# Kernel tuning notes

Measured on AMD Instinct MI355X. Metric: run time of the kernel, lower is better.

## Reference

```python
import jax, jax.numpy as jnp
import numpy as np
from jax import lax

H = 2048          # hidden_size
NAH = 16          # num attn heads
AHD = H // NAH    # 128
NFH = 4           # num lact (fast-weight) heads
FHD = H // NFH    # 512 = d_in = d_out
DH = FHD          # d_h = d_in * inter_multi (1.0)
WIN = 1024        # sliding window
CHUNK = 512       # lact chunk size
B, S = 2, 2048
ROPE_BASE = 500000.0
EPS = 1e-6
BASE_LR_INV = 0.001 + float(np.log(-np.expm1(-0.001)))  # inv_softplus(1e-3)


def rms_norm(x, w):
    return x * lax.rsqrt(jnp.mean(x * x, axis=-1, keepdims=True) + EPS) * w


def silu(x):
    return x * jax.nn.sigmoid(x)


def silu_backprop(dy, x):
    sg = jax.nn.sigmoid(x)
    return dy * sg * (1.0 + x * (1.0 - sg))


def apply_rope(q, k):
    # q,k: [b,s,h,d]; non-interleaved (half-split) rotary, matching flash-attn RotaryEmbedding
    d = q.shape[-1]
    inv_freq = 1.0 / (ROPE_BASE ** (jnp.arange(0, d, 2, dtype=jnp.float32) / d))
    t = jnp.arange(q.shape[1], dtype=jnp.float32)
    freqs = jnp.outer(t, inv_freq)                       # [s, d/2]
    cos = jnp.cos(freqs)[None, :, None, :]
    sin = jnp.sin(freqs)[None, :, None, :]
    def rot(x):
        x1, x2 = jnp.split(x, 2, axis=-1)
        return jnp.concatenate([x1 * cos - x2 * sin, x2 * cos + x1 * sin], axis=-1)
    return rot(q), rot(k)


def sliding_window_attn(q, k, v):
    # [b,s,h,d]; causal sliding-window attention
    s = q.shape[1]
    scale = 1.0 / np.sqrt(q.shape[-1])
    i = jnp.arange(s)[:, None]
    j = jnp.arange(s)[None, :]
    mask = (j <= i) & (i - j < WIN)                      # [s,s]
    scores = jnp.einsum('bihd,bjhd->bhij', q, k) * scale
    scores = jnp.where(mask[None, None], scores, -jnp.inf)
    p = jax.nn.softmax(scores, axis=-1)
    return jnp.einsum('bhij,bjhd->bihd', p, v)


def setup_inputs() -> dict:
    key = jax.random.key(0)
    ks = jax.random.split(key, 10)
    def n(k, shape, scale):
        return jax.random.normal(k, shape, dtype=jnp.float32) * scale
    return {
        'hidden_states': n(ks[0], (B, S, H), 1.0),
        'attn_qkv_w': n(ks[1], (3 * H, H), 0.02),
        'attn_o_w': n(ks[2], (H, H), 0.02),
        'q_norm_w': jnp.ones((H,), jnp.float32),
        'k_norm_w': jnp.ones((H,), jnp.float32),
        'mlp_norm_w': jnp.ones((H,), jnp.float32),
        'mlp_qkv_w': n(ks[3], (3 * NFH * FHD, H), 0.02),
        'mlp_o_w': n(ks[4], (H, NFH * FHD), 0.02),
        'lr_w': n(ks[5], (3 * NFH, H), 0.02),
        'lr_b': jnp.zeros((3 * NFH,), jnp.float32),
        'w0': n(ks[6], (NFH, DH, FHD), 1.0 / np.sqrt(FHD)),
        'w1': n(ks[7], (NFH, FHD, DH), 1.0 / np.sqrt(DH)),
        'w2': n(ks[8], (NFH, DH, FHD), 1.0 / np.sqrt(FHD)),
        'ttt_norm_w': jnp.ones((FHD,), jnp.float32),
    }


def _forward(hidden_states, attn_qkv_w, attn_o_w, q_norm_w, k_norm_w, mlp_norm_w,
             mlp_qkv_w, mlp_o_w, lr_w, lr_b, w0, w1, w2, ttt_norm_w):
    b, s, _ = hidden_states.shape
    # ---- sliding window attention (token mixer) ----
    qkv = hidden_states @ attn_qkv_w.T
    q, k, v = jnp.split(qkv, 3, axis=-1)
    q = rms_norm(q, q_norm_w)
    k = rms_norm(k, k_norm_w)
    q = q.reshape(b, s, NAH, AHD)
    k = k.reshape(b, s, NAH, AHD)
    v = v.reshape(b, s, NAH, AHD)
    q, k = apply_rope(q, k)
    o = sliding_window_attn(q, k, v)
    attn_out = o.reshape(b, s, H) @ attn_o_w.T

    # ---- TTT-MLP SwiGLU fast-weight channel mixer after SWA ----
    x = rms_norm(attn_out, mlp_norm_w)
    fqkv = x @ mlp_qkv_w.T
    fq, fk, fv = jnp.split(fqkv, 3, axis=-1)
    fq, fk, fv = silu(fq), silu(fk), silu(fv)
    fq = fq.reshape(b, s, NFH, FHD)
    fk = fk.reshape(b, s, NFH, FHD)
    fv = fv.reshape(b, s, NFH, FHD)
    fq = fq / jnp.clip(jnp.linalg.norm(fq, axis=-1, keepdims=True), 1e-6)
    fk = fk / jnp.clip(jnp.linalg.norm(fk, axis=-1, keepdims=True), 1e-6)

    # per-token lrs (mamba parameterization: softplus(proj + inv_softplus(base_lr)))
    lr = jax.nn.softplus(x @ lr_w.T + lr_b + BASE_LR_INV)   # [b,s,3*NFH]
    l0, l1, l2 = jnp.split(lr, 3, axis=-1)                  # each [b,s,NFH]

    nc = s // CHUNK
    def chunkify(t):  # [b,s,h,d] -> [nc,b,h,c,d]
        return t.reshape(b, nc, CHUNK, t.shape[2], t.shape[3]).transpose(1, 0, 3, 2, 4)
    qs = chunkify(fq)
    ks_ = chunkify(fk)
    vs = chunkify(fv)
    l0s = chunkify(l0[..., None])
    l1s = chunkify(l1[..., None])
    l2s = chunkify(l2[..., None])

    w0b = jnp.broadcast_to(w0[None], (b,) + w0.shape)
    w1b = jnp.broadcast_to(w1[None], (b,) + w1.shape)
    w2b = jnp.broadcast_to(w2[None], (b,) + w2.shape)

    def step(carry, inp):
        cw0, cw1, cw2 = carry
        qc, kc, vc, lr0, lr1, lr2 = inp   # qc/kc/vc: [b,h,c,d]; lr*: [b,h,c,1]
        # apply current fast weights to queries of this chunk (apply-then-update)
        gq = jnp.einsum('bhed,bhcd->bhce', cw0, qc)
        hq = silu(gq) * jnp.einsum('bhed,bhcd->bhce', cw2, qc)
        oc = jnp.einsum('bhoe,bhce->bhco', cw1, hq)
        # update fast weights with this chunk's (k, v) under negative dot-product loss
        gk = jnp.einsum('bhed,bhcd->bhce', cw0, kc)      # gate pre-act
        hbm = jnp.einsum('bhed,bhcd->bhce', cw2, kc)     # hidden before mul
        hid = silu(gk) * hbm
        dhid = jnp.einsum('bhoe,bhco->bhce', cw1, vc)    # grad wrt hidden
        dhbm = dhid * silu(gk)
        dgate = dhid * hbm
        dgpre = silu_backprop(dgate, gk)
        nw1 = cw1 + jnp.einsum('bhco,bhce->bhoe', vc * lr1, hid)
        nw0 = cw0 + jnp.einsum('bhce,bhcd->bhed', dgpre, kc * lr0)
        nw2 = cw2 + jnp.einsum('bhce,bhcd->bhed', dhbm, kc * lr2)
        return (nw0, nw1, nw2), oc

    _, ocs = lax.scan(step, (w0b, w1b, w2b), (qs, ks_, vs, l0s, l1s, l2s))
    o_fw = ocs.transpose(1, 0, 3, 2, 4).reshape(b, s, NFH, FHD)
    o_fw = rms_norm(o_fw, ttt_norm_w)
    ttt_out = o_fw.reshape(b, s, NFH * FHD) @ mlp_o_w.T
    return attn_out + ttt_out


def reference(hidden_states, attn_qkv_w, attn_o_w, q_norm_w, k_norm_w, mlp_norm_w,
              mlp_qkv_w, mlp_o_w, lr_w, lr_b, w0, w1, w2, ttt_norm_w):
    return _forward(hidden_states, attn_qkv_w, attn_o_w, q_norm_w, k_norm_w, mlp_norm_w,
                    mlp_qkv_w, mlp_o_w, lr_w, lr_b, w0, w1, w2, ttt_norm_w)
```

## Files before the change

### kernel.cpp

```cpp
#include <hip/hip_runtime.h>
#include <cmath>

typedef unsigned short u16;
typedef unsigned int u32;
typedef short s16x8 __attribute__((ext_vector_type(8)));
typedef short s16x4 __attribute__((ext_vector_type(4)));
typedef float f32x4 __attribute__((ext_vector_type(4)));

#define DEV static __device__ __forceinline__

DEV float b2f(u16 h) { return __uint_as_float(((u32)h) << 16); }
DEV u16 f2b(float f) {
  u32 u = __float_as_uint(f);
  u = (u + 0x7FFFu + ((u >> 16) & 1u)) >> 16;
  return (u16)u;
}
DEV float siluf(float x) { return x / (1.f + __expf(-x)); }

DEV void gload16(const void* g, void* l) {
  __builtin_amdgcn_global_load_lds((const __attribute__((address_space(1))) void*)g,
                                   (__attribute__((address_space(3))) void*)l, 16, 0, 0);
}

DEV s16x8 lds_frag(const u16* buf, int row, int kg) {
  int lin = row * 64 + kg * 16;
  int adr = lin ^ (((row >> 1) & 3) << 4);
  return *(const s16x8*)((const char*)buf + adr);
}

template <int MODE>
__global__ __launch_bounds__(256, 3) void gemm128(const u16* __restrict__ A, const u16* __restrict__ B,
                                                  void* __restrict__ Cout, const float* __restrict__ Cin,
                                                  int ldc, int K, int gx) {
  __shared__ __align__(16) u16 Al[3][128 * 32];
  __shared__ __align__(16) u16 Bl[3][128 * 32];
  int tid = threadIdx.x, w = tid >> 6, l = tid & 63;
  int cpx = gx >> 3;
  int idx = blockIdx.x >> 3;
  int bx = (blockIdx.x & 7) * cpx + idx % cpx;
  int by = idx / cpx;
  const u16* Ab = A + (long)by * 128 * K;
  const u16* Bb = B + (long)bx * 128 * K;
  int wr = w >> 1, wc = w & 1;
  int fro = l & 15, kg = l >> 4;
  f32x4 acc[4][4] = {};
  int nk = K >> 5;

  auto stage = [&](int buf, int kt) {
    #pragma unroll
    for (int i = 0; i < 2; ++i) {
      int x = (tid + i * 256) * 16;
      int y = x ^ (((x >> 7) & 3) << 4);
      gload16(Ab + (long)(y >> 6) * K + kt * 32 + ((y & 63) >> 1), (char*)&Al[buf][0] + x);
      gload16(Bb + (long)(y >> 6) * K + kt * 32 + ((y & 63) >> 1), (char*)&Bl[buf][0] + x);
    }
  };

  stage(0, 0);
  stage(1, 1);
  asm volatile("s_waitcnt vmcnt(4)" ::: "memory");
  __builtin_amdgcn_s_barrier();

  int cur = 0;
  for (int t = 0; t < nk; ++t) {
    const u16* Ac = &Al[cur][0];
    const u16* Bc = &Bl[cur][0];
    s16x8 af[4], bfr[4];
    #pragma unroll
    for (int m = 0; m < 4; ++m) af[m] = lds_frag(Ac, wr * 64 + m * 16 + fro, kg);
    #pragma unroll
    for (int n = 0; n < 4; ++n) bfr[n] = lds_frag(Bc, wc * 64 + n * 16 + fro, kg);
    if (t + 2 < nk) {
      int nb = cur + 2; if (nb >= 3) nb -= 3;
      stage(nb, t + 2);
    }
    __builtin_amdgcn_s_setprio(1);
    #pragma unroll
    for (int m = 0; m < 4; ++m)
      #pragma unroll
      for (int n = 0; n < 4; ++n)
        acc[m][n] = __builtin_amdgcn_mfma_f32_16x16x32_bf16(af[m], bfr[n], acc[m][n], 0, 0, 0);
    __builtin_amdgcn_s_setprio(0);
    if (t + 2 < nk)      asm volatile("s_waitcnt vmcnt(4)" ::: "memory");
    else if (t + 1 < nk) asm volatile("s_waitcnt vmcnt(0)" ::: "memory");
    __builtin_amdgcn_s_barrier();
    if (++cur == 3) cur = 0;
  }

  long rbase = (long)by * 128 + wr * 64 + kg * 4;
  long cbase = (long)bx * 128 + wc * 64 + fro;
  #pragma unroll
  for (int m = 0; m < 4; ++m)
    #pragma unroll
    for (int n = 0; n < 4; ++n)
      #pragma unroll
      for (int j = 0; j < 4; ++j) {
        long r = rbase + m * 16 + j;
        long c = cbase + n * 16;
        float v = acc[m][n][j];
        if (MODE == 2) v += Cin[r * ldc + c];
        if (MODE == 0) ((u16*)Cout)[r * ldc + c] = f2b(v);
        else ((float*)Cout)[r * ldc + c] = v;
      }
}

struct GemmDesc {
  const u16* A; const u16* B;
  float* C; const float* Cin;
  u16* Cb; u16* CbT;
  long sAb, sAh, sBb, sBh, sCb_, sCh_, sCbb, sCbh, sCtb, sCth;
  int lda, ldb, ldc, ldcb, ldct, K;
};
struct GemmBatch { GemmDesc d[5]; int nbh; };

__global__ __launch_bounds__(256) void gemm_bt(GemmBatch gb) {
  int di = blockIdx.z / gb.nbh;
  int bh = blockIdx.z % gb.nbh;
  GemmDesc d = gb.d[di];
  __shared__ __align__(16) u16 As[2][4096];
  __shared__ __align__(16) u16 Bs[2][4096];
  int tid = threadIdx.x, w = tid >> 6, l = tid & 63;
  int b2 = bh >> 2, h2 = bh & 3;
  const u16* Ab = d.A + (long)b2 * d.sAb + (long)h2 * d.sAh + (long)blockIdx.y * 128 * d.lda;
  const u16* Bb = d.B + (long)b2 * d.sBb + (long)h2 * d.sBh + (long)blockIdx.x * 128 * d.ldb;
  int srow = l >> 2, scol = (l & 3) * 8;
  f32x4 acc[4][4] = {};
  int nk = d.K >> 5;

  auto stage = [&](int buf, int kt) {
    #pragma unroll
    for (int i = 0; i < 2; ++i) {
      int chunk = i * 4 + w;
      int row = chunk * 16 + srow;
      gload16(Ab + (long)row * d.lda + kt * 32 + scol, &As[buf][chunk * 512]);
      gload16(Bb + (long)row * d.ldb + kt * 32 + scol, &Bs[buf][chunk * 512]);
    }
  };

  stage(0, 0);
  asm volatile("s_waitcnt vmcnt(0)" ::: "memory");
  __syncthreads();

  int wr = (w >> 1) * 64, wc = (w & 1) * 64;
  int fro = l & 15, fko = (l >> 4) * 8;

  for (int kt = 0; kt < nk; ++kt) {
    int buf = kt & 1;
    if (kt + 1 < nk) stage(buf ^ 1, kt + 1);
    s16x8 af[4], bfr[4];
    #pragma unroll
    for (int m = 0; m < 4; ++m) af[m] = *(const s16x8*)&As[buf][(wr + m * 16 + fro) * 32 + fko];
    #pragma unroll
    for (int n = 0; n < 4; ++n) bfr[n] = *(const s16x8*)&Bs[buf][(wc + n * 16 + fro) * 32 + fko];
    #pragma unroll
    for (int m = 0; m < 4; ++m)
      #pragma unroll
      for (int n = 0; n < 4; ++n)
        acc[m][n] = __builtin_amdgcn_mfma_f32_16x16x32_bf16(af[m], bfr[n], acc[m][n], 0, 0, 0);
    asm volatile("s_waitcnt vmcnt(0)" ::: "memory");
    __syncthreads();
  }

  float* Cp = d.C ? d.C + (long)b2 * d.sCb_ + (long)h2 * d.sCh_ : nullptr;
  const float* Ci = d.Cin ? d.Cin + (long)b2 * d.sCb_ + (long)h2 * d.sCh_ : nullptr;
  u16* Cbp = d.Cb ? d.Cb + (long)b2 * d.sCbb + (long)h2 * d.sCbh : nullptr;
  u16* Ctp = d.CbT ? d.CbT + (long)b2 * d.sCtb + (long)h2 * d.sCth : nullptr;
  long rbase = (long)blockIdx.y * 128 + wr + (l >> 4) * 4;
  long cbase = (long)blockIdx.x * 128 + wc + (l & 15);
  #pragma unroll
  for (int m = 0; m < 4; ++m)
    #pragma unroll
    for (int n = 0; n < 4; ++n)
      #pragma unroll
      for (int j = 0; j < 4; ++j) {
        long r = rbase + m * 16 + j;
        long c = cbase + n * 16;
        float v = acc[m][n][j];
        if (Ci) v += Ci[r * d.ldc + c];
        if (Cp) Cp[r * d.ldc + c] = v;
        if (Cbp) Cbp[r * d.ldcb + c] = f2b(v);
        if (Ctp) Ctp[c * d.ldct + r] = f2b(v);
      }
}

__global__ __launch_bounds__(256) void convk(const float* __restrict__ in, u16* __restrict__ outp) {
  long i = ((long)blockIdx.x * 256 + threadIdx.x) * 4;
  float4 v = *(const float4*)(in + i);
  u16 o[4] __attribute__((aligned(8))) = {f2b(v.x), f2b(v.y), f2b(v.z), f2b(v.w)};
  *(s16x4*)&outp[i] = *(const s16x4*)o;
}

__global__ __launch_bounds__(256) void norm_rope_kernel(const u16* __restrict__ qkv,
    const float* __restrict__ qw, const float* __restrict__ kw,
    u16* __restrict__ qg, u16* __restrict__ kg, u16* __restrict__ vg) {
  __shared__ float qsh[2048], ksh[2048];
  __shared__ float red[2][4];
  int t = blockIdx.x, tid = threadIdx.x, w = tid >> 6, l = tid & 63;
  int s = t & 2047;
  const u16* row = qkv + (long)t * 6144;
  s16x8 vq = *(const s16x8*)&row[tid * 8];
  s16x8 vk = *(const s16x8*)&row[2048 + tid * 8];
  float sq = 0.f, sk = 0.f;
  #pragma unroll
  for (int i = 0; i < 8; ++i) {
    float a = b2f((u16)vq[i]); qsh[tid * 8 + i] = a; sq += a * a;
    float c = b2f((u16)vk[i]); ksh[tid * 8 + i] = c; sk += c * c;
  }
  *(s16x8*)&vg[(long)t * 2048 + tid * 8] = *(const s16x8*)&row[4096 + tid * 8];
  #pragma unroll
  for (int mk = 32; mk; mk >>= 1) { sq += __shfl_xor(sq, mk, 64); sk += __shfl_xor(sk, mk, 64); }
  if (l == 0) { red[0][w] = sq; red[1][w] = sk; }
  __syncthreads();
  float rq = rsqrtf((red[0][0] + red[0][1] + red[0][2] + red[0][3]) * (1.f / 2048.f) + 1e-6f);
  float rk = rsqrtf((red[1][0] + red[1][1] + red[1][2] + red[1][3]) * (1.f / 2048.f) + 1e-6f);
  const float lf = 13.122363377404329f / 64.f;
  #pragma unroll
  for (int ii = 0; ii < 4; ++ii) {
    int pid = tid + 256 * ii;
    int h = pid >> 6, dpos = pid & 63;
    float invf = expf(-(float)dpos * lf);
    float ang = (float)s * invf;
    float sn, cs;
    sincosf(ang, &sn, &cs);
    int i1 = h * 128 + dpos, i2 = i1 + 64;
    float q1 = qsh[i1] * rq * qw[i1], q2 = qsh[i2] * rq * qw[i2];
    qg[(long)t * 2048 + i1] = f2b(q1 * cs - q2 * sn);
    qg[(long)t * 2048 + i2] = f2b(q2 * cs + q1 * sn);
    float k1 = ksh[i1] * rk * kw[i1], k2v = ksh[i2] * rk * kw[i2];
    kg[(long)t * 2048 + i1] = f2b(k1 * cs - k2v * sn);
    kg[(long)t * 2048 + i2] = f2b(k2v * cs + k1 * sn);
  }
}

__global__ __launch_bounds__(256) void vtrans_kernel(const u16* __restrict__ v, u16* __restrict__ vT) {
  __shared__ u16 T[64][74];
  int tid = threadIdx.x;
  int bh = blockIdx.z, b = bh >> 4, h = bh & 15;
  int ts = blockIdx.x * 64, dg = blockIdx.y * 64;
  int r = tid >> 2, c0 = (tid & 3) * 16;
  const u16* src = v + ((long)b * 2048 + ts + r) * 2048 + h * 128 + dg + c0;
  *(s16x8*)&T[r][c0] = *(const s16x8*)src;
  *(s16x8*)&T[r][c0 + 8] = *(const s16x8*)(src + 8);
  __syncthreads();
  int d = tid >> 2, tg = (tid & 3) * 16;
  u16 a[16] __attribute__((aligned(16)));
  #pragma unroll
  for (int j = 0; j < 16; ++j) a[j] = T[tg + j][d];
  u16* dst = vT + ((long)bh * 128 + dg + d) * 2048 + ts + tg;
  *(s16x8*)dst = ((const s16x8*)a)[0];
  *(s16x8*)(dst + 8) = ((const s16x8*)a)[1];
}

__global__ __launch_bounds__(256, 3) void attn_kernel(const u16* __restrict__ qg, const u16* __restrict__ kg,
                                                      const u16* __restrict__ vT, u16* __restrict__ og) {
  __shared__ __align__(16) u16 Ks[64][136];
  __shared__ __align__(16) u16 Vt[128][72];
  __shared__ __align__(16) u16 Ps[4][16][72];
  int tid = threadIdx.x, w = tid >> 6, l = tid & 63;
  int h = blockIdx.y, b = blockIdx.z;
  int qs = blockIdx.x * 64;
  long tokb = (long)b * 2048;
  int fr = l & 15, fg = l >> 4;
  int wrow = qs + w * 16;

  s16x8 qf[4];
  #pragma unroll
  for (int ks = 0; ks < 4; ++ks)
    qf[ks] = *(const s16x8*)&qg[(tokb + wrow + fr) * 2048 + h * 128 + ks * 32 + fg * 8];

  f32x4 oacc[8] = {};
  float mrun[4], lrun[4];
  #pragma unroll
  for (int j = 0; j < 4; ++j) { mrun[j] = -__builtin_inff(); lrun[j] = 0.f; }

  int lo = qs - 1023;
  int t0 = lo > 0 ? (lo >> 6) : 0;
  int t1 = (qs + 63) >> 6;
  const float scale = 0.088388347648318447f;

  const u16* kbase = kg + tokb * 2048 + h * 128;
  const u16* vbase = vT + (long)(b * 16 + h) * 128 * 2048;

  s16x8 kreg[4], vreg[4];
  auto loadrg = [&](int kvs) {
    #pragma unroll
    for (int it = 0; it < 4; ++it) {
      int idx = it * 256 + tid;
      kreg[it] = *(const s16x8*)&kbase[(long)(kvs + (idx >> 4)) * 2048 + (idx & 15) * 8];
      vreg[it] = *(const s16x8*)&vbase[(long)(idx >> 3) * 2048 + kvs + (idx & 7) * 8];
    }
  };
  auto writelds = [&]() {
    #pragma unroll
    for (int it = 0; it < 4; ++it) {
      int idx = it * 256 + tid;
      *(s16x8*)&Ks[idx >> 4][(idx & 15) * 8] = kreg[it];
      *(s16x8*)&Vt[idx >> 3][(idx & 7) * 8] = vreg[it];
    }
  };

  loadrg(t0 << 6);
  writelds();
  __syncthreads();

  for (int kt = t0; kt <= t1; ++kt) {
    int kvs = kt << 6;
    if (kt < t1) loadrg((kt + 1) << 6);
    bool active = (kvs <= wrow + 15);
    if (active) {
      f32x4 st[4] = {};
      #pragma unroll
      for (int ct = 0; ct < 4; ++ct)
        #pragma unroll
        for (int ks = 0; ks < 4; ++ks) {
          s16x8 kf = *(const s16x8*)&Ks[ct * 16 + fr][ks * 32 + fg * 8];
          st[ct] = __builtin_amdgcn_mfma_f32_16x16x32_bf16(qf[ks], kf, st[ct], 0, 0, 0);
        }
      bool needm = (kvs + 63 > wrow) || (kvs < wrow - 1008);
      float mx[4];
      #pragma unroll
      for (int j = 0; j < 4; ++j) mx[j] = -__builtin_inff();
      #pragma unroll
      for (int ct = 0; ct < 4; ++ct)
        #pragma unroll
        for (int j = 0; j < 4; ++j) {
          float s = st[ct][j] * scale;
          if (needm) {
            int r = wrow + fg * 4 + j;
            int c = kvs + ct * 16 + fr;
            if (c > r || (r - c) >= 1024) s = -__builtin_inff();
          }
          st[ct][j] = s;
          mx[j] = fmaxf(mx[j], s);
        }
      #pragma unroll
      for (int mk = 8; mk; mk >>= 1)
        #pragma unroll
        for (int j = 0; j < 4; ++j) mx[j] = fmaxf(mx[j], __shfl_xor(mx[j], mk, 64));
      float sc[4], nmu[4], rs[4];
      #pragma unroll
      for (int j = 0; j < 4; ++j) {
        float nm = fmaxf(mrun[j], mx[j]);
        nmu[j] = (nm == -__builtin_inff()) ? 0.f : nm;
        sc[j] = __expf(mrun[j] - nmu[j]);
        mrun[j] = nm;
        rs[j] = 0.f;
      }
      #pragma unroll
      for (int ct = 0; ct < 4; ++ct)
        #pragma unroll
        for (int j = 0; j < 4; ++j) {
          float p = __expf(st[ct][j] - nmu[j]);
          rs[j] += p;
          Ps[w][fg * 4 + j][ct * 16 + fr] = f2b(p);
        }
      #pragma unroll
      for (int mk = 8; mk; mk >>= 1)
        #pragma unroll
        for (int j = 0; j < 4; ++j) rs[j] += __shfl_xor(rs[j], mk, 64);
      #pragma unroll
      for (int j = 0; j < 4; ++j) lrun[j] = lrun[j] * sc[j] + rs[j];
      #pragma unroll
      for (int dt = 0; dt < 8; ++dt)
        #pragma unroll
        for (int j = 0; j < 4; ++j) oacc[dt][j] *= sc[j];
      #pragma unroll
      for (int kst = 0; kst < 2; ++kst) {
        s16x8 pf = *(const s16x8*)&Ps[w][fr][kst * 32 + fg * 8];
        #pragma unroll
        for (int dt = 0; dt < 8; ++dt) {
          s16x8 vf = *(const s16x8*)&Vt[dt * 16 + fr][kst * 32 + fg * 8];
          oacc[dt] = __builtin_amdgcn_mfma_f32_16x16x32_bf16(pf, vf, oacc[dt], 0, 0, 0);
        }
      }
    }
    __syncthreads();
    if (kt < t1) {
      writelds();
    }
    __syncthreads();
  }
  #pragma unroll
  for (int j = 0; j < 4; ++j) {
    float inv = 1.f / lrun[j];
    long rofs = (tokb + wrow + fg * 4 + j) * 2048 + h * 128;
    #pragma unroll
    for (int dt = 0; dt < 8; ++dt)
      og[rofs + dt * 16 + fr] = f2b(oacc[dt][j] * inv);
  }
}

__global__ __launch_bounds__(256) void rms_x_kernel(const float* __restrict__ src, const float* __restrict__ wgt,
                                                    u16* __restrict__ dst) {
  __shared__ float red[4];
  int t = blockIdx.x, tid = threadIdx.x, w = tid >> 6, l = tid & 63;
  const float* row = src + (long)t * 2048;
  float v[8] __attribute__((aligned(16)));
  ((float4*)v)[0] = *(const float4*)&row[tid * 8];
  ((float4*)v)[1] = *(const float4*)&row[tid * 8 + 4];
  float ss = 0.f;
  #pragma unroll
  for (int i = 0; i < 8; ++i) ss += v[i] * v[i];
  #pragma unroll
  for (int mk = 32; mk; mk >>= 1) ss += __shfl_xor(ss, mk, 64);
  if (l == 0) red[w] = ss;
  __syncthreads();
  float r = rsqrtf((red[0] + red[1] + red[2] + red[3]) * (1.f / 2048.f) + 1e-6f);
  #pragma unroll
  for (int i = 0; i < 8; ++i) dst[(long)t * 2048 + tid * 8 + i] = f2b(v[i] * r * wgt[tid * 8 + i]);
}

__global__ __launch_bounds__(256) void lr_kernel(const u16* __restrict__ xb, const float* __restrict__ lrw,
                                                 const float* __restrict__ lrbias, float* __restrict__ lrout,
                                                 float base) {
  __shared__ float red[4][12];
  int t = blockIdx.x, tid = threadIdx.x, w = tid >> 6, l = tid & 63;
  float xv[8];
  s16x8 rv = *(const s16x8*)&xb[(long)t * 2048 + tid * 8];
  #pragma unroll
  for (int i = 0; i < 8; ++i) xv[i] = b2f((u16)rv[i]);
  float acc[12];
  #pragma unroll
  for (int j = 0; j < 12; ++j) {
    const float4* w4 = (const float4*)(lrw + j * 2048 + tid * 8);
    float4 a = w4[0], bq = w4[1];
    acc[j] = xv[0] * a.x + xv[1] * a.y + xv[2] * a.z + xv[3] * a.w +
             xv[4] * bq.x + xv[5] * bq.y + xv[6] * bq.z + xv[7] * bq.w;
  }
  #pragma unroll
  for (int j = 0; j < 12; ++j)
    #pragma unroll
    for (int mk = 32; mk; mk >>= 1) acc[j] += __shfl_xor(acc[j], mk, 64);
  if (l == 0) {
    #pragma unroll
    for (int j = 0; j < 12; ++j) red[w][j] = acc[j];
  }
  __syncthreads();
  if (tid < 12) {
    float s_ = red[0][tid] + red[1][tid] + red[2][tid] + red[3][tid] + lrbias[tid] + base;
    lrout[(long)t * 12 + tid] = (s_ > 20.f) ? s_ : log1pf(__expf(s_));
  }
}

__global__ __launch_bounds__(256) void silu_norm_kernel(const u16* __restrict__ fqkv,
    u16* __restrict__ fqo, u16* __restrict__ fko, u16* __restrict__ fvo) {
  int t = blockIdx.x, tid = threadIdx.x, w = tid >> 6, l = tid & 63;
  const u16* row = fqkv + (long)t * 6144;
  {
    s16x8 rv = *(const s16x8*)&row[w * 512 + l * 8];
    float x[8]; float ss = 0.f;
    #pragma unroll
    for (int i = 0; i < 8; ++i) { x[i] = siluf(b2f((u16)rv[i])); ss += x[i] * x[i]; }
    #pragma unroll
    for (int mk = 32; mk; mk >>= 1) ss += __shfl_xor(ss, mk, 64);
    float sc = 1.f / fmaxf(sqrtf(ss), 1e-6f);
    #pragma unroll
    for (int i = 0; i < 8; ++i) fqo[(long)t * 2048 + w * 512 + l * 8 + i] = f2b(x[i] * sc);
  }
  {
    s16x8 rv = *(const s16x8*)&row[2048 + w * 512 + l * 8];
    float x[8]; float ss = 0.f;
    #pragma unroll
    for (int i = 0; i < 8; ++i) { x[i] = siluf(b2f((u16)rv[i])); ss += x[i] * x[i]; }
    #pragma unroll
    for (int mk = 32; mk; mk >>= 1) ss += __shfl_xor(ss, mk, 64);
    float sc = 1.f / fmaxf(sqrtf(ss), 1e-6f);
    #pragma unroll
    for (int i = 0; i < 8; ++i) fko[(long)t * 2048 + w * 512 + l * 8 + i] = f2b(x[i] * sc);
  }
  {
    s16x8 rv = *(const s16x8*)&row[4096 + tid * 8];
    #pragma unroll
    for (int i = 0; i < 8; ++i) fvo[(long)t * 2048 + tid * 8 + i] = f2b(siluf(b2f((u16)rv[i])));
  }
}

__global__ __launch_bounds__(256) void winit_kernel(const float* __restrict__ w0, const float* __restrict__ w1,
                                                    const float* __restrict__ w2,
                                                    float* __restrict__ wbuf0, u16* __restrict__ wb16) {
  long gid = (long)blockIdx.x * 256 + threadIdx.x;
  long e4 = gid * 4;
  int which = (int)(e4 >> 21);
  long rem = e4 & 2097151L;
  int bh = (int)(rem >> 18);
  long idx = rem & 262143L;
  int h = bh & 3;
  const float* src = (which == 0 ? w0 : which == 1 ? w1 : w2) + (long)h * 262144 + idx;
  float4 v = *(const float4*)src;
  *(float4*)(wbuf0 + e4) = v;
  u16 o[4] __attribute__((aligned(8))) = {f2b(v.x), f2b(v.y), f2b(v.z), f2b(v.w)};
  *(s16x4*)&wb16[e4] = *(const s16x4*)o;
  if (which == 1) {
    u16* wt = wb16 + 3L * 2097152 + (long)bh * 262144;
    int r = (int)(idx >> 9), c = (int)(idx & 511);
    wt[(long)(c + 0) * 512 + r] = o[0];
    wt[(long)(c + 1) * 512 + r] = o[1];
    wt[(long)(c + 2) * 512 + r] = o[2];
    wt[(long)(c + 3) * 512 + r] = o[3];
  }
}

__global__ __launch_bounds__(256) void ttt_elem_kernel(
    const float* __restrict__ t5, u16* __restrict__ hqb,
    u16* __restrict__ hidT, u16* __restrict__ dhbmT, u16* __restrict__ dgpT,
    const u16* __restrict__ fk, const u16* __restrict__ fv, const float* __restrict__ lr,
    u16* __restrict__ k0T, u16* __restrict__ k2T, u16* __restrict__ v1T, int ic) {
  __shared__ u16 T0[64][72], T1[64][72], T2[64][72];
  int tid = threadIdx.x;
  int bh = blockIdx.y, b = bh >> 2, h = bh & 3;
  int tc = (blockIdx.x >> 3) * 64, te = (blockIdx.x & 7) * 64;
  int r = tid >> 2, c0 = (tid & 3) * 16;
  long base = (long)bh * 262144 + (long)(tc + r) * 512 + te + c0;

  {
    float gq_[16] __attribute__((aligned(16)));
    float q2_[16] __attribute__((aligned(16)));
    const float* pgq = t5 + base;
    const float* pq2 = t5 + 2097152L + base;
    #pragma unroll
    for (int q4 = 0; q4 < 4; ++q4) {
      ((float4*)gq_)[q4] = *(const float4*)(pgq + q4 * 4);
      ((float4*)q2_)[q4] = *(const float4*)(pq2 + q4 * 4);
    }
    u16 hq_[16] __attribute__((aligned(16)));
    #pragma unroll
    for (int i = 0; i < 16; ++i) hq_[i] = f2b(siluf(gq_[i]) * q2_[i]);
    *(s16x8*)&hqb[base] = ((const s16x8*)hq_)[0];
    *(s16x8*)&hqb[base + 8] = ((const s16x8*)hq_)[1];
  }
  {
    float gk_[16] __attribute__((aligned(16)));
    float k2_[16] __attribute__((aligned(16)));
    float dh_[16] __attribute__((aligned(16)));
    const float* pgk = t5 + 2L * 2097152 + base;
    const float* pk2 = t5 + 3L * 2097152 + base;
    const float* pdh = t5 + 4L * 2097152 + base;
    #pragma unroll
    for (int q4 = 0; q4 < 4; ++q4) {
      ((float4*)gk_)[q4] = *(const float4*)(pgk + q4 * 4);
      ((float4*)k2_)[q4] = *(const float4*)(pk2 + q4 * 4);
      ((float4*)dh_)[q4] = *(const float4*)(pdh + q4 * 4);
    }
    #pragma unroll
    for (int i = 0; i < 16; ++i) {
      float sg = 1.f / (1.f + __expf(-gk_[i]));
      float sil = gk_[i] * sg;
      float hid = sil * k2_[i];
      float dhbm = dh_[i] * sil;
      float dgate = dh_[i] * k2_[i];
      float dgp = dgate * sg * (1.f + gk_[i] * (1.f - sg));
      T0[r][c0 + i] = f2b(hid);
      T1[r][c0 + i] = f2b(dhbm);
      T2[r][c0 + i] = f2b(dgp);
    }
  }
  __syncthreads();
  long obase = (long)bh * 262144 + (long)(te + r) * 512 + tc + c0;
  {
    u16 a0[16] __attribute__((aligned(16))), a1[16] __attribute__((aligned(16))), a2[16] __attribute__((aligned(16)));
    #pragma unroll
    for (int i = 0; i < 16; ++i) { a0[i] = T0[c0 + i][r]; a1[i] = T1[c0 + i][r]; a2[i] = T2[c0 + i][r]; }
    *(s16x8*)&hidT[obase] = ((const s16x8*)a0)[0];   *(s16x8*)&hidT[obase + 8] = ((const s16x8*)a0)[1];
    *(s16x8*)&dhbmT[obase] = ((const s16x8*)a1)[0];  *(s16x8*)&dhbmT[obase + 8] = ((const s16x8*)a1)[1];
    *(s16x8*)&dgpT[obase] = ((const s16x8*)a2)[0];   *(s16x8*)&dgpT[obase + 8] = ((const s16x8*)a2)[1];
  }
  __syncthreads();
  {
    long to = (long)b * 2048 + (long)ic * 512 + tc + r;
    float l0 = lr[to * 12 + h], l1 = lr[to * 12 + 4 + h], l2 = lr[to * 12 + 8 + h];
    long goff = to * 2048 + (long)h * 512 + te + c0;
    s16x8 ka = *(const s16x8*)&fk[goff];
    s16x8 kb8 = *(const s16x8*)&fk[goff + 8];
    s16x8 va = *(const s16x8*)&fv[goff];
    s16x8 vb8 = *(const s16x8*)&fv[goff + 8];
    #pragma unroll
    for (int i = 0; i < 8; ++i) {
      float kv1 = b2f((u16)ka[i]), kv2 = b2f((u16)kb8[i]);
      float vv1 = b2f((u16)va[i]), vv2 = b2f((u16)vb8[i]);
      T0[r][c0 + i] = f2b(kv1 * l0);      T0[r][c0 + 8 + i] = f2b(kv2 * l0);
      T1[r][c0 + i] = f2b(kv1 * l2);      T1[r][c0 + 8 + i] = f2b(kv2 * l2);
      T2[r][c0 + i] = f2b(vv1 * l1);      T2[r][c0 + 8 + i] = f2b(vv2 * l1);
    }
  }
  __syncthreads();
  {
    u16 a0[16] __attribute__((aligned(16))), a1[16] __attribute__((aligned(16))), a2[16] __attribute__((aligned(16)));
    #pragma unroll
    for (int i = 0; i < 16; ++i) { a0[i] = T0[c0 + i][r]; a1[i] = T1[c0 + i][r]; a2[i] = T2[c0 + i][r]; }
    *(s16x8*)&k0T[obase] = ((const s16x8*)a0)[0];  *(s16x8*)&k0T[obase + 8] = ((const s16x8*)a0)[1];
    *(s16x8*)&k2T[obase] = ((const s16x8*)a1)[0];  *(s16x8*)&k2T[obase + 8] = ((const s16x8*)a1)[1];
    *(s16x8*)&v1T[obase] = ((const s16x8*)a2)[0];  *(s16x8*)&v1T[obase + 8] = ((const s16x8*)a2)[1];
  }
}

__global__ __launch_bounds__(256) void ttt_norm_kernel(const u16* __restrict__ src, const float* __restrict__ wgt,
                                                       u16* __restrict__ dst) {
  int t = blockIdx.x, tid = threadIdx.x, w = tid >> 6, l = tid & 63;
  long off = (long)t * 2048 + w * 512 + l * 8;
  s16x8 rv = *(const s16x8*)&src[off];
  float x[8];
  float ss = 0.f;
  #pragma unroll
  for (int i = 0; i < 8; ++i) { x[i] = b2f((u16)rv[i]); ss += x[i] * x[i]; }
  #pragma unroll
  for (int mk = 32; mk; mk >>= 1) ss += __shfl_xor(ss, mk, 64);
  float r = rsqrtf(ss * (1.f / 512.f) + 1e-6f);
  #pragma unroll
  for (int i = 0; i < 8; ++i) dst[off + i] = f2b(x[i] * r * wgt[l * 8 + i]);
}

extern "C" void kernel_launch(void* const* d_in, const int* in_sizes, int n_in,
                              void* d_out, int out_size, void* d_ws, size_t ws_size,
                              hipStream_t stream) {
  const float* hidden     = (const float*)d_in[0];
  const float* attn_qkv_w = (const float*)d_in[1];
  const float* attn_o_w   = (const float*)d_in[2];
  const float* q_norm_w   = (const float*)d_in[3];
  const float* k_norm_w   = (const float*)d_in[4];
  const float* mlp_norm_w = (const float*)d_in[5];
  const float* mlp_qkv_w  = (const float*)d_in[6];
  const float* mlp_o_w    = (const float*)d_in[7];
  const float* lr_w       = (const float*)d_in[8];
  const float* lr_bias    = (const float*)d_in[9];
  const float* w0in       = (const float*)d_in[10];
  const float* w1in       = (const float*)d_in[11];
  const float* w2in       = (const float*)d_in[12];
  const float* ttt_w      = (const float*)d_in[13];
  float* out = (float*)d_out;

  char* ws = (char*)d_ws;
  u16* hbf   = (u16*)(ws + 0);
  u16* wqb   = (u16*)(ws + 16777216);
  u16* wob   = (u16*)(ws + 41943040);
  char* big  = ws + 50331648;
  u16* qbuf  = (u16*)(ws + 121634816);
  u16* kbuf  = (u16*)(ws + 138412032);
  u16* vbuf  = (u16*)(ws + 155189248);
  u16* obuf  = (u16*)(ws + 171966464);
  float* lrb_ = (float*)(ws + 188743680);
  float* wbuf = (float*)(ws + 188940288);
  u16* wb16  = (u16*)(ws + 239271936);

  u16* qkvb = (u16*)big;
  u16* vTb  = (u16*)(big + 50331648);
  float* t5 = (float*)big;
  u16* hqb   = (u16*)(big + 41943040);
  u16* hidT  = (u16*)(big + 46137344);
  u16* dhbmT = (u16*)(big + 50331648);
  u16* dgpT  = (u16*)(big + 54525952);
  u16* k0T   = (u16*)(big + 58720256);
  u16* k2T   = (u16*)(big + 62914560);
  u16* v1T   = (u16*)(big + 67108864);
  u16* xb  = hbf;
  u16* ofw = hbf;

  convk<<<8192, 256, 0, stream>>>(hidden, hbf);
  convk<<<12288, 256, 0, stream>>>(attn_qkv_w, wqb);
  convk<<<4096, 256, 0, stream>>>(attn_o_w, wob);

  gemm128<0><<<1536, 256, 0, stream>>>(hbf, wqb, qkvb, nullptr, 6144, 2048, 48);
  norm_rope_kernel<<<4096, 256, 0, stream>>>(qkvb, q_norm_w, k_norm_w, qbuf, kbuf, vbuf);
  vtrans_kernel<<<dim3(32, 2, 32), 256, 0, stream>>>(vbuf, vTb);
  attn_kernel<<<dim3(32, 16, 2), 256, 0, stream>>>(qbuf, kbuf, vTb, obuf);
  gemm128<1><<<512, 256, 0, stream>>>(obuf, wob, out, nullptr, 2048, 2048, 16);
  rms_x_kernel<<<4096, 256, 0, stream>>>(out, mlp_norm_w, xb);
  convk<<<12288, 256, 0, stream>>>(mlp_qkv_w, wqb);
  convk<<<4096, 256, 0, stream>>>(mlp_o_w, wob);
  float base_lr_inv = 0.001f + logf(-expm1f(-0.001f));
  lr_kernel<<<4096, 256, 0, stream>>>(xb, lr_w, lr_bias, lrb_, base_lr_inv);
  gemm128<0><<<1536, 256, 0, stream>>>(xb, wqb, qkvb, nullptr, 6144, 2048, 48);
  silu_norm_kernel<<<4096, 256, 0, stream>>>(qkvb, qbuf, kbuf, vbuf);
  winit_kernel<<<6144, 256, 0, stream>>>(w0in, w1in, w2in, wbuf, wb16);

  for (int ic = 0; ic < 4; ++ic) {
    {
      GemmBatch g{}; g.nbh = 8;
      const u16* Asrc[5] = {qbuf, qbuf, kbuf, kbuf, vbuf};
      long Bwhich[5] = {0, 2, 0, 2, 3};
      for (int i = 0; i < 5; ++i) {
        GemmDesc& dd = g.d[i];
        dd.A = Asrc[i] + (long)ic * 1048576; dd.sAb = 4194304; dd.sAh = 512; dd.lda = 2048;
        dd.B = wb16 + Bwhich[i] * 2097152;   dd.sBb = 1048576; dd.sBh = 262144; dd.ldb = 512;
        dd.C = t5 + (long)i * 2097152;       dd.sCb_ = 1048576; dd.sCh_ = 262144; dd.ldc = 512;
        dd.K = 512;
      }
      gemm_bt<<<dim3(4, 4, 40), 256, 0, stream>>>(g);
    }
    ttt_elem_kernel<<<dim3(64, 8), 256, 0, stream>>>(t5, hqb, hidT, dhbmT, dgpT,
                                                     kbuf, vbuf, lrb_, k0T, k2T, v1T, ic);
    {
      GemmBatch g{}; g.nbh = 8;
      GemmDesc& dd = g.d[0];
      dd.A = hqb; dd.sAb = 1048576; dd.sAh = 262144; dd.lda = 512;
      dd.B = wb16 + 2097152; dd.sBb = 1048576; dd.sBh = 262144; dd.ldb = 512;
      dd.Cb = ofw + (long)ic * 1048576; dd.sCbb = 4194304; dd.sCbh = 512; dd.ldcb = 2048;
      dd.K = 512;
      gemm_bt<<<dim3(4, 4, 8), 256, 0, stream>>>(g);
    }
    {
      GemmBatch g{}; g.nbh = 8;
      float* wc_ = wbuf + (long)(ic & 1) * 6291456;
      float* wn_ = wbuf + (long)((ic & 1) ^ 1) * 6291456;
      const u16* A3[3] = {dgpT, v1T, dhbmT};
      const u16* B3[3] = {k0T, hidT, k2T};
      for (int i = 0; i < 3; ++i) {
        GemmDesc& dd = g.d[i];
        dd.A = A3[i]; dd.sAb = 1048576; dd.sAh = 262144; dd.lda = 512;
        dd.B = B3[i]; dd.sBb = 1048576; dd.sBh = 262144; dd.ldb = 512;
        dd.Cin = wc_ + (long)i * 2097152; dd.C = wn_ + (long)i * 2097152;
        dd.sCb_ = 1048576; dd.sCh_ = 262144; dd.ldc = 512;
        dd.Cb = wb16 + (long)i * 2097152; dd.sCbb = 1048576; dd.sCbh = 262144; dd.ldcb = 512;
        if (i == 1) { dd.CbT = wb16 + 3L * 2097152; dd.sCtb = 1048576; dd.sCth = 262144; dd.ldct = 512; }
        dd.K = 512;
      }
      gemm_bt<<<dim3(4, 4, 24), 256, 0, stream>>>(g);
    }
  }
  ttt_norm_kernel<<<4096, 256, 0, stream>>>(ofw, ttt_w, obuf);
  gemm128<2><<<512, 256, 0, stream>>>(obuf, wob, out, out, 2048, 2048, 16);
  (void)in_sizes; (void)n_in; (void)out_size; (void)ws_size;
}
```

Measured before the change: 994.3 us.

## Triple-buffer swizzled LDS in batched GEMM and double attention query tile

The batched fast-weight GEMM moves from a double-buffered to a triple-buffered LDS pipeline. It uses an XOR-swizzled layout read through lds_frag, partial vmcnt waits with raw barriers, and raised priority around the MFMA block, aiming to hide global-load latency and cut LDS bank conflicts. The sliding-window attention kernel now processes 128 query rows per block (32 per wave) instead of 64, so each K/V tile loaded into LDS is reused across twice as many queries. A reordered block index balances causal work across blocks. The costs are more registers and LDS per block, lower occupancy bounds, and more masked waste on diagonal tiles.

```diff
diff --git a/kernel.cpp b/kernel.cpp
--- a/kernel.cpp
+++ b/kernel.cpp
@@ -113,60 +113,69 @@
 };
 struct GemmBatch { GemmDesc d[5]; int nbh; };
 
-__global__ __launch_bounds__(256) void gemm_bt(GemmBatch gb) {
+__global__ __launch_bounds__(256, 3) void gemm_bt(GemmBatch gb) {
   int di = blockIdx.z / gb.nbh;
   int bh = blockIdx.z % gb.nbh;
   GemmDesc d = gb.d[di];
-  __shared__ __align__(16) u16 As[2][4096];
-  __shared__ __align__(16) u16 Bs[2][4096];
+  __shared__ __align__(16) u16 As[3][4096];
+  __shared__ __align__(16) u16 Bs[3][4096];
   int tid = threadIdx.x, w = tid >> 6, l = tid & 63;
   int b2 = bh >> 2, h2 = bh & 3;
   const u16* Ab = d.A + (long)b2 * d.sAb + (long)h2 * d.sAh + (long)blockIdx.y * 128 * d.lda;
   const u16* Bb = d.B + (long)b2 * d.sBb + (long)h2 * d.sBh + (long)blockIdx.x * 128 * d.ldb;
-  int srow = l >> 2, scol = (l & 3) * 8;
   f32x4 acc[4][4] = {};
   int nk = d.K >> 5;
 
   auto stage = [&](int buf, int kt) {
     #pragma unroll
     for (int i = 0; i < 2; ++i) {
-      int chunk = i * 4 + w;
-      int row = chunk * 16 + srow;
-      gload16(Ab + (long)row * d.lda + kt * 32 + scol, &As[buf][chunk * 512]);
-      gload16(Bb + (long)row * d.ldb + kt * 32 + scol, &Bs[buf][chunk * 512]);
+      int x = (tid + i * 256) * 16;
+      int y = x ^ (((x >> 7) & 3) << 4);
+      gload16(Ab + (long)(y >> 6) * d.lda + kt * 32 + ((y & 63) >> 1), (char*)&As[buf][0] + x);
+      gload16(Bb + (long)(y >> 6) * d.ldb + kt * 32 + ((y & 63) >> 1), (char*)&Bs[buf][0] + x);
     }
   };
 
   stage(0, 0);
-  asm volatile("s_waitcnt vmcnt(0)" ::: "memory");
-  __syncthreads();
+  stage(1, 1);
+  asm volatile("s_waitcnt vmcnt(4)" ::: "memory");
+  __builtin_amdgcn_s_barrier();
 
   int wr = (w >> 1) * 64, wc = (w & 1) * 64;
-  int fro = l & 15, fko = (l >> 4) * 8;
-
+  int fro = l & 15, kg = l >> 4;
+
+  int cur = 0;
   for (int kt = 0; kt < nk; ++kt) {
-    int buf = kt & 1;
-    if (kt + 1 < nk) stage(buf ^ 1, kt + 1);
+    const u16* Ac = &As[cur][0];
+    const u16* Bc = &Bs[cur][0];
     s16x8 af[4], bfr[4];
     #pragma unroll
-    for (int m = 0; m < 4; ++m) af[m] = *(const s16x8*)&As[buf][(wr + m * 16 + fro) * 32 + fko];
-    #pragma unroll
-    for (int n = 0; n < 4; ++n) bfr[n] = *(const s16x8*)&Bs[buf][(wc + n * 16 + fro) * 32 + fko];
+    for (int m = 0; m < 4; ++m) af[m] = lds_frag(Ac, wr + m * 16 + fro, kg);
+    #pragma unroll
+    for (int n = 0; n < 4; ++n) bfr[n] = lds_frag(Bc, wc + n * 16 + fro, kg);
+    if (kt + 2 < nk) {
+      int nb = cur + 2; if (nb >= 3) nb -= 3;
+      stage(nb, kt + 2);
+    }
+    __builtin_amdgcn_s_setprio(1);
     #pragma unroll
     for (int m = 0; m < 4; ++m)
       #pragma unroll
       for (int n = 0; n < 4; ++n)
         acc[m][n] = __builtin_amdgcn_mfma_f32_16x16x32_bf16(af[m], bfr[n], acc[m][n], 0, 0, 0);
-    asm volatile("s_waitcnt vmcnt(0)" ::: "memory");
-    __syncthreads();
+    __builtin_amdgcn_s_setprio(0);
+    if (kt + 2 < nk)      asm volatile("s_waitcnt vmcnt(4)" ::: "memory");
+    else if (kt + 1 < nk) asm volatile("s_waitcnt vmcnt(0)" ::: "memory");
+    __builtin_amdgcn_s_barrier();
+    if (++cur == 3) cur = 0;
   }
 
   float* Cp = d.C ? d.C + (long)b2 * d.sCb_ + (long)h2 * d.sCh_ : nullptr;
   const float* Ci = d.Cin ? d.Cin + (long)b2 * d.sCb_ + (long)h2 * d.sCh_ : nullptr;
   u16* Cbp = d.Cb ? d.Cb + (long)b2 * d.sCbb + (long)h2 * d.sCbh : nullptr;
   u16* Ctp = d.CbT ? d.CbT + (long)b2 * d.sCtb + (long)h2 * d.sCth : nullptr;
-  long rbase = (long)blockIdx.y * 128 + wr + (l >> 4) * 4;
-  long cbase = (long)blockIdx.x * 128 + wc + (l & 15);
+  long rbase = (long)blockIdx.y * 128 + wr + kg * 4;
+  long cbase = (long)blockIdx.x * 128 + wc + fro;
   #pragma unroll
   for (int m = 0; m < 4; ++m)
     #pragma unroll
@@ -251,31 +260,36 @@
   *(s16x8*)(dst + 8) = ((const s16x8*)a)[1];
 }
 
-__global__ __launch_bounds__(256, 3) void attn_kernel(const u16* __restrict__ qg, const u16* __restrict__ kg,
+__global__ __launch_bounds__(256, 2) void attn_kernel(const u16* __restrict__ qg, const u16* __restrict__ kg,
                                                       const u16* __restrict__ vT, u16* __restrict__ og) {
   __shared__ __align__(16) u16 Ks[64][136];
   __shared__ __align__(16) u16 Vt[128][72];
-  __shared__ __align__(16) u16 Ps[4][16][72];
+  __shared__ __align__(16) u16 Ps[4][32][72];
   int tid = threadIdx.x, w = tid >> 6, l = tid & 63;
   int h = blockIdx.y, b = blockIdx.z;
-  int qs = blockIdx.x * 64;
+  int xs = ((blockIdx.x & 7) << 1) | (blockIdx.x >> 3);
+  int qs = xs * 128;
   long tokb = (long)b * 2048;
   int fr = l & 15, fg = l >> 4;
-  int wrow = qs + w * 16;
-
-  s16x8 qf[4];
-  #pragma unroll
-  for (int ks = 0; ks < 4; ++ks)
-    qf[ks] = *(const s16x8*)&qg[(tokb + wrow + fr) * 2048 + h * 128 + ks * 32 + fg * 8];
-
-  f32x4 oacc[8] = {};
-  float mrun[4], lrun[4];
-  #pragma unroll
-  for (int j = 0; j < 4; ++j) { mrun[j] = -__builtin_inff(); lrun[j] = 0.f; }
+  int wrow = qs + w * 32;
+
+  s16x8 qf[2][4];
+  #pragma unroll
+  for (int rt = 0; rt < 2; ++rt)
+    #pragma unroll
+    for (int ks = 0; ks < 4; ++ks)
+      qf[rt][ks] = *(const s16x8*)&qg[(tokb + wrow + rt * 16 + fr) * 2048 + h * 128 + ks * 32 + fg * 8];
+
+  f32x4 oacc[2][8] = {};
+  float mrun[2][4], lrun[2][4];
+  #pragma unroll
+  for (int rt = 0; rt < 2; ++rt)
+    #pragma unroll
+    for (int j = 0; j < 4; ++j) { mrun[rt][j] = -__builtin_inff(); lrun[rt][j] = 0.f; }
 
   int lo = qs - 1023;
   int t0 = lo > 0 ? (lo >> 6) : 0;
-  int t1 = (qs + 63) >> 6;
+  int t1 = (qs + 127) >> 6;
   const float scale = 0.088388347648318447f;
 
   const u16* kbase = kg + tokb * 2048 + h * 128;
@@ -306,71 +320,77 @@
   for (int kt = t0; kt <= t1; ++kt) {
     int kvs = kt << 6;
     if (kt < t1) loadrg((kt + 1) << 6);
-    bool active = (kvs <= wrow + 15);
+    bool active = (kvs <= wrow + 31);
     if (active) {
-      f32x4 st[4] = {};
+      f32x4 st[2][4] = {};
       #pragma unroll
       for (int ct = 0; ct < 4; ++ct)
         #pragma unroll
         for (int ks = 0; ks < 4; ++ks) {
           s16x8 kf = *(const s16x8*)&Ks[ct * 16 + fr][ks * 32 + fg * 8];
-          st[ct] = __builtin_amdgcn_mfma_f32_16x16x32_bf16(qf[ks], kf, st[ct], 0, 0, 0);
+          st[0][ct] = __builtin_amdgcn_mfma_f32_16x16x32_bf16(qf[0][ks], kf, st[0][ct], 0, 0, 0);
+          st[1][ct] = __builtin_amdgcn_mfma_f32_16x16x32_bf16(qf[1][ks], kf, st[1][ct], 0, 0, 0);
         }
-      bool needm = (kvs + 63 > wrow) || (kvs < wrow - 1008);
-      float mx[4];
+      bool needm = (kvs + 63 > wrow) || (kvs < wrow - 992);
       #pragma unroll
-      for (int j = 0; j < 4; ++j) mx[j] = -__builtin_inff();
-      #pragma unroll
-      for (int ct = 0; ct < 4; ++ct)
+      for (int rt = 0; rt < 2; ++rt) {
+        float mx[4];
+        #pragma unroll
+        for (int j = 0; j < 4; ++j) mx[j] = -__builtin_inff();
+        #pragma unroll
+        for (int ct = 0; ct < 4; ++ct)
+          #pragma unroll
+          for (int j = 0; j < 4; ++j) {
+            float s = st[rt][ct][j] * scale;
+            if (needm) {
+              int r = wrow + rt * 16 + fg * 4 + j;
+              int c = kvs + ct * 16 + fr;
+              if (c > r || (r - c) >= 1024) s = -__builtin_inff();
+            }
+            st[rt][ct][j] = s;
+            mx[j] = fmaxf(mx[j], s);
+          }
+        #pragma unroll
+        for (int mk = 8; mk; mk >>= 1)
+          #pragma unroll
+          for (int j = 0; j < 4; ++j) mx[j] = fmaxf(mx[j], __shfl_xor(mx[j], mk, 64));
+        float sc[4], nmu[4], rs[4];
         #pragma unroll
         for (int j = 0; j < 4; ++j) {
-          float s = st[ct][j] * scale;
-          if (needm) {
-            int r = wrow + fg * 4 + j;
-            int c = kvs + ct * 16 + fr;
-            if (c > r || (r - c) >= 1024) s = -__builtin_inff();
+          float nm = fmaxf(mrun[rt][j], mx[j]);
+          nmu[j] = (nm == -__builtin_inff()) ? 0.f : nm;
+          sc[j] = __expf(mrun[rt][j] - nmu[j]);
+          mrun[rt][j] = nm;
+          rs[j] = 0.f;
+        }
+        #pragma unroll
+        for (int ct = 0; ct < 4; ++ct)
+          #pragma unroll
+          for (int j = 0; j < 4; ++j) {
+            float p = __expf(st[rt][ct][j] - nmu[j]);
+            rs[j] += p;
+            Ps[w][rt * 16 + fg * 4 + j][ct * 16 + fr] = f2b(p);
           }
-          st[ct][j] = s;
-          mx[j] = fmaxf(mx[j], s);
-        }
-      #pragma unroll
-      for (int mk = 8; mk; mk >>= 1)
-        #pragma unroll
-        for (int j = 0; j < 4; ++j) mx[j] = fmaxf(mx[j], __shfl_xor(mx[j], mk, 64));
-      float sc[4], nmu[4], rs[4];
-      #pragma unroll
-      for (int j = 0; j < 4; ++j) {
-        float nm = fmaxf(mrun[j], mx[j]);
-        nmu[j] = (nm == -__builtin_inff()) ? 0.f : nm;
-        sc[j] = __expf(mrun[j] - nmu[j]);
-        mrun[j] = nm;
-        rs[j] = 0.f;
+        #pragma unroll
+        for (int mk = 8; mk; mk >>= 1)
+          #pragma unroll
+          for (int j = 0; j < 4; ++j) rs[j] += __shfl_xor(rs[j], mk, 64);
+        #pragma unroll
+        for (int j = 0; j < 4; ++j) lrun[rt][j] = lrun[rt][j] * sc[j] + rs[j];
+        #pragma unroll
+        for (int dt = 0; dt < 8; ++dt)
+          #pragma unroll
+          for (int j = 0; j < 4; ++j) oacc[rt][dt][j] *= sc[j];
       }
       #pragma unroll
-      for (int ct = 0; ct < 4; ++ct)
-        #pragma unroll
-        for (int j = 0; j < 4; ++j) {
-          float p = __expf(st[ct][j] - nmu[j]);
-          rs[j] += p;
-          Ps[w][fg * 4 + j][ct * 16 + fr] = f2b(p);
-        }
-      #pragma unroll
-      for (int mk = 8; mk; mk >>= 1)
-        #pragma unroll
-        for (int j = 0; j < 4; ++j) rs[j] += __shfl_xor(rs[j], mk, 64);
-      #pragma unroll
-      for (int j = 0; j < 4; ++j) lrun[j] = lrun[j] * sc[j] + rs[j];
-      #pragma unroll
-      for (int dt = 0; dt < 8; ++dt)
-        #pragma unroll
-        for (int j = 0; j < 4; ++j) oacc[dt][j] *= sc[j];
-      #pragma unroll
       for (int kst = 0; kst < 2; ++kst) {
-        s16x8 pf = *(const s16x8*)&Ps[w][fr][kst * 32 + fg * 8];
+        s16x8 pf0 = *(const s16x8*)&Ps[w][fr][kst * 32 + fg * 8];
+        s16x8 pf1 = *(const s16x8*)&Ps[w][16 + fr][kst * 32 + fg * 8];
         #pragma unroll
         for (int dt = 0; dt < 8; ++dt) {
           s16x8 vf = *(const s16x8*)&Vt[dt * 16 + fr][kst * 32 + fg * 8];
-          oacc[dt] = __builtin_amdgcn_mfma_f32_16x16x32_bf16(pf, vf, oacc[dt], 0, 0, 0);
+          oacc[0][dt] = __builtin_amdgcn_mfma_f32_16x16x32_bf16(pf0, vf, oacc[0][dt], 0, 0, 0);
+          oacc[1][dt] = __builtin_amdgcn_mfma_f32_16x16x32_bf16(pf1, vf, oacc[1][dt], 0, 0, 0);
         }
       }
     }
@@ -381,13 +401,15 @@
     __syncthreads();
   }
   #pragma unroll
-  for (int j = 0; j < 4; ++j) {
-    float inv = 1.f / lrun[j];
-    long rofs = (tokb + wrow + fg * 4 + j) * 2048 + h * 128;
-    #pragma unroll
-    for (int dt = 0; dt < 8; ++dt)
-      og[rofs + dt * 16 + fr] = f2b(oacc[dt][j] * inv);
-  }
+  for (int rt = 0; rt < 2; ++rt)
+    #pragma unroll
+    for (int j = 0; j < 4; ++j) {
+      float inv = 1.f / lrun[rt][j];
+      long rofs = (tokb + wrow + rt * 16 + fg * 4 + j) * 2048 + h * 128;
+      #pragma unroll
+      for (int dt = 0; dt < 8; ++dt)
+        og[rofs + dt * 16 + fr] = f2b(oacc[rt][dt][j] * inv);
+    }
 }
 
 __global__ __launch_bounds__(256) void rms_x_kernel(const float* __restrict__ src, const float* __restrict__ wgt,
@@ -661,7 +683,7 @@
   gemm128<0><<<1536, 256, 0, stream>>>(hbf, wqb, qkvb, nullptr, 6144, 2048, 48);
   norm_rope_kernel<<<4096, 256, 0, stream>>>(qkvb, q_norm_w, k_norm_w, qbuf, kbuf, vbuf);
   vtrans_kernel<<<dim3(32, 2, 32), 256, 0, stream>>>(vbuf, vTb);
-  attn_kernel<<<dim3(32, 16, 2), 256, 0, stream>>>(qbuf, kbuf, vTb, obuf);
+  attn_kernel<<<dim3(16, 16, 2), 256, 0, stream>>>(qbuf, kbuf, vTb, obuf);
   gemm128<1><<<512, 256, 0, stream>>>(obuf, wob, out, nullptr, 2048, 2048, 16);
   rms_x_kernel<<<4096, 256, 0, stream>>>(out, mlp_norm_w, xb);
   convk<<<12288, 256, 0, stream>>>(mlp_qkv_w, wqb);
```

Result: faster. 959.8 us (-3.5%).
